# Kernel tuning notes

Hardware: AMD Instinct MI355X
Metric: run time of the kernel (lower is better)

## Reference

```python
import jax, jax.numpy as jnp
import numpy as np

N = 100000
E = 1600000
D = 128  # in_dim == out_dim


def setup_inputs() -> dict:
    key = jax.random.key(0)
    k1, k2, k3, k4, k5 = jax.random.split(key, 5)
    x = jax.random.normal(k1, (N, D), dtype=jnp.float32)
    edge_index = jax.random.randint(k2, (2, E), 0, N, dtype=jnp.int64)
    edge_attr = jax.random.normal(k3, (E, 8), dtype=jnp.float32)
    # nn.Linear(in_dim, out_dim) params: W [out, in], b [out]
    bound = 1.0 / np.sqrt(D)
    W = jax.random.uniform(k4, (D, D), minval=-bound, maxval=bound, dtype=jnp.float32)
    b = jax.random.uniform(k5, (D,), minval=-bound, maxval=bound, dtype=jnp.float32)
    return {"x": x, "edge_index": edge_index, "edge_attr": edge_attr, "W": W, "b": b}


def reference(x, edge_index, edge_attr, W, b):
    row, col = edge_index[0], edge_index[1]
    # gather neighbor features then scatter-add into destination rows
    agg = jax.ops.segment_sum(x[col], row, num_segments=x.shape[0])  # [N, D]
    h = (x + agg) @ W.T + b  # linear
    return jax.nn.silu(h)
```

## Files before the change

### kernel.cpp

```cpp
#include <hip/hip_runtime.h>
#include <math.h>

#define NN 100000
#define NE 1600000
#define DD 128
#define CAP 64

#define NB    512
#define CHUNK 3125
#define QCAP  768

typedef short bf16x8 __attribute__((ext_vector_type(8)));
typedef float f32x4  __attribute__((ext_vector_type(4)));

__device__ inline float bf2f(unsigned short u) {
    unsigned int v = ((unsigned int)u) << 16;
    return __uint_as_float(v);
}
__device__ inline unsigned short f2bf(float f) {
    unsigned int u = __float_as_uint(f);
    unsigned int r = (u + 0x7FFFu + ((u >> 16) & 1u)) >> 16;
    return (unsigned short)r;
}

__global__ void f2bf_kernel(const float* __restrict__ src,
                            unsigned short* __restrict__ dst, int n4) {
    int i = blockIdx.x * blockDim.x + threadIdx.x;
    if (i >= n4) return;
    float4 v = ((const float4*)src)[i];
    ushort4 o;
    o.x = f2bf(v.x); o.y = f2bf(v.y); o.z = f2bf(v.z); o.w = f2bf(v.w);
    ((ushort4*)dst)[i] = o;
}

__global__ void zero_cnt_kernel(int* cnt) {
    int i = blockIdx.x * blockDim.x + threadIdx.x;
    if (i < NN) cnt[i] = 0;
}

__global__ __launch_bounds__(256)
void partition_kernel(const int* __restrict__ eidx,
                      unsigned long long* __restrict__ q,
                      int* __restrict__ qn) {
    __shared__ int qc[8];
    if (threadIdx.x < 8) qc[threadIdx.x] = 0;
    __syncthreads();
    const int base = blockIdx.x * CHUNK;
    for (int i = threadIdx.x; i < CHUNK; i += 256) {
        const int e = base + i;
        const int r = __builtin_nontemporal_load(&eidx[e]);
        const int c = __builtin_nontemporal_load(&eidx[NE + e]);
        const int b = r / 12500;
        const int pos = atomicAdd(&qc[b], 1);
        if (pos < QCAP)
            q[((size_t)blockIdx.x * 8 + b) * QCAP + pos] =
                ((unsigned long long)(unsigned)c << 32) | (unsigned)r;
    }
    __syncthreads();
    if (threadIdx.x < 8) {
        int v = qc[threadIdx.x]; if (v > QCAP) v = QCAP;
        qn[blockIdx.x * 8 + threadIdx.x] = v;
    }
}

__global__ __launch_bounds__(256)
void scatter_kernel(const unsigned long long* __restrict__ q,
                    const int* __restrict__ qn,
                    int* __restrict__ cnt,
                    int* __restrict__ slot) {
    const int bucket = blockIdx.x & 7;
    const int chunk  = blockIdx.x >> 3;
    const int n = qn[chunk * 8 + bucket];
    const unsigned long long* qq = q + ((size_t)chunk * 8 + bucket) * QCAP;
    for (int i = threadIdx.x; i < n; i += 256) {
        const unsigned long long p = qq[i];
        const int r = (int)(p & 0xffffffffu);
        const int c = (int)(p >> 32);
        const int pos = atomicAdd(&cnt[r], 1);
        if (pos < CAP) slot[(r << 6) + pos] = c;
    }
}

__global__ __launch_bounds__(256)
void gather_kernel(const unsigned short* __restrict__ x16,
                   const int* __restrict__ cnt,
                   const int* __restrict__ slot,
                   unsigned short* __restrict__ V16) {
    const int lane = threadIdx.x & 15;
    const int node = (int)((blockIdx.x * 256u + threadIdx.x) >> 4);
    if (node >= NN) return;
    const bf16x8* xv = (const bf16x8*)x16;

    bf16x8 s = xv[(size_t)node * 16 + lane];
    float a[8];
    #pragma unroll
    for (int k = 0; k < 8; ++k) a[k] = bf2f((unsigned short)s[k]);

    int deg = cnt[node];
    if (deg > CAP) deg = CAP;
    const int base = node << 6;

    for (int d = 0; d < deg; d += 8) {
        const int4 c0 = *(const int4*)&slot[base + d];
        const int4 c1 = *(const int4*)&slot[base + d + 4];
        int idx[8] = {c0.x, c0.y, c0.z, c0.w, c1.x, c1.y, c1.z, c1.w};
        float w[8];
        #pragma unroll
        for (int j = 0; j < 8; ++j) {
            const bool live = (d + j) < deg;
            w[j] = live ? 1.f : 0.f;
            if (!live) idx[j] = node;
        }
        bf16x8 t[8];
        #pragma unroll
        for (int j = 0; j < 8; ++j) t[j] = xv[(size_t)idx[j] * 16 + lane];
        #pragma unroll
        for (int j = 0; j < 8; ++j) {
            #pragma unroll
            for (int k = 0; k < 8; ++k)
                a[k] = fmaf(w[j], bf2f((unsigned short)t[j][k]), a[k]);
        }
    }

    bf16x8 o;
    #pragma unroll
    for (int k = 0; k < 8; ++k) o[k] = (short)f2bf(a[k]);
    ((bf16x8*)V16)[(size_t)node * 16 + lane] = o;
}

__global__ __launch_bounds__(256)
void gemm_mfma_kernel(const unsigned short* __restrict__ V16,
                      const unsigned short* __restrict__ W16,
                      const float* __restrict__ bias,
                      float* __restrict__ out) {
    const int wave = threadIdx.x >> 6;
    const int lane = threadIdx.x & 63;
    const int strip = blockIdx.x * 4 + wave;
    if (strip >= NN / 16) return;
    const int m0 = strip << 4;
    const int r = lane & 15;
    const int q = lane >> 4;

    const bf16x8* Arow = (const bf16x8*)(V16 + (size_t)(m0 + r) * 128);
    bf16x8 a[4];
    #pragma unroll
    for (int kk = 0; kk < 4; ++kk) a[kk] = Arow[kk * 4 + q];

    f32x4 acc[8];
    #pragma unroll
    for (int n = 0; n < 8; ++n) acc[n] = (f32x4){0.f, 0.f, 0.f, 0.f};

    #pragma unroll
    for (int kk = 0; kk < 4; ++kk) {
        #pragma unroll
        for (int n = 0; n < 8; ++n) {
            const bf16x8 b =
                ((const bf16x8*)(W16 + (size_t)(n * 16 + r) * 128))[kk * 4 + q];
            acc[n] = __builtin_amdgcn_mfma_f32_16x16x32_bf16(a[kk], b, acc[n], 0, 0, 0);
        }
    }

    #pragma unroll
    for (int n = 0; n < 8; ++n) {
        const int col = n * 16 + r;
        const float bv = bias[col];
        #pragma unroll
        for (int i = 0; i < 4; ++i) {
            const int row = m0 + q * 4 + i;
            float h = acc[n][i] + bv;
            h = h / (1.f + __expf(-h));
            out[(size_t)row * 128 + col] = h;
        }
    }
}

extern "C" void kernel_launch(void* const* d_in, const int* in_sizes, int n_in,
                              void* d_out, int out_size, void* d_ws, size_t ws_size,
                              hipStream_t stream) {
    const float* x    = (const float*)d_in[0];
    const int*   eidx = (const int*)d_in[1];
    const float* W    = (const float*)d_in[3];
    const float* b    = (const float*)d_in[4];
    float* out = (float*)d_out;

    char* ws = (char*)d_ws;
    int*            cnt  = (int*)(ws);
    int*            qn   = (int*)(ws + (448u << 10));
    int*            slot = (int*)(ws + (512u << 10));
    unsigned short* x16  = (unsigned short*)(ws + (26u << 20));
    unsigned short* V16  = (unsigned short*)(ws + (51u << 20));
    unsigned short* W16  = (unsigned short*)(ws + (76u << 20));
    unsigned long long* q = (unsigned long long*)(ws + (51u << 20));

    zero_cnt_kernel<<<(NN + 255) / 256, 256, 0, stream>>>(cnt);
    partition_kernel<<<NB, 256, 0, stream>>>(eidx, q, qn);
    scatter_kernel<<<8 * NB, 256, 0, stream>>>(q, qn, cnt, slot);
    f2bf_kernel<<<(NN * DD / 4 + 255) / 256, 256, 0, stream>>>(x, x16, NN * DD / 4);
    f2bf_kernel<<<(DD * DD / 4 + 255) / 256, 256, 0, stream>>>(W, W16, DD * DD / 4);
    gather_kernel<<<(NN * 16 + 255) / 256, 256, 0, stream>>>(x16, cnt, slot, V16);
    gemm_mfma_kernel<<<(NN / 16 + 3) / 4, 256, 0, stream>>>(V16, W16, b, out);
}
```

Before: 329.4 us.

## Fuse adjacency build into gather using per-block shared-memory buckets

Partitions edges into 512 fine-grained destination buckets, with an overflow list for buckets that exceed their per-chunk capacity. A single fused kernel then builds each bucket's adjacency lists in LDS with shared atomics and immediately performs the neighbor gather. This removes the global count/slot arrays, the zeroing kernel and the global-atomic scatter pass. In exchange, only 512 blocks of 512 threads do the gather, each using about 50KB of LDS, which lowers occupancy and parallelism in the gather phase. Every block also scans the whole overflow list.

```diff
diff --git a/kernel.cpp b/kernel.cpp
--- a/kernel.cpp
+++ b/kernel.cpp
@@ -6,9 +6,12 @@
 #define DD 128
 #define CAP 64
 
-#define NB    512
-#define CHUNK 3125
-#define QCAP  768
+#define NB     64
+#define CHUNK  25000
+#define NBUCK  512
+#define BNODES 196
+#define QCAP2  96
+#define OVCAP  8192
 
 typedef short bf16x8 __attribute__((ext_vector_type(8)));
 typedef float f32x4  __attribute__((ext_vector_type(4)));
@@ -33,99 +36,124 @@
     ((ushort4*)dst)[i] = o;
 }
 
-__global__ void zero_cnt_kernel(int* cnt) {
-    int i = blockIdx.x * blockDim.x + threadIdx.x;
-    if (i < NN) cnt[i] = 0;
-}
+__global__ void zero_ovn_kernel(int* ovn) { *ovn = 0; }
 
 __global__ __launch_bounds__(256)
 void partition_kernel(const int* __restrict__ eidx,
                       unsigned long long* __restrict__ q,
-                      int* __restrict__ qn) {
-    __shared__ int qc[8];
-    if (threadIdx.x < 8) qc[threadIdx.x] = 0;
+                      int* __restrict__ qn,
+                      unsigned long long* __restrict__ ovf,
+                      int* __restrict__ ovn) {
+    __shared__ int qc[NBUCK];
+    for (int i = threadIdx.x; i < NBUCK; i += 256) qc[i] = 0;
     __syncthreads();
     const int base = blockIdx.x * CHUNK;
     for (int i = threadIdx.x; i < CHUNK; i += 256) {
         const int e = base + i;
         const int r = __builtin_nontemporal_load(&eidx[e]);
         const int c = __builtin_nontemporal_load(&eidx[NE + e]);
-        const int b = r / 12500;
+        const int b = r / BNODES;
         const int pos = atomicAdd(&qc[b], 1);
-        if (pos < QCAP)
-            q[((size_t)blockIdx.x * 8 + b) * QCAP + pos] =
-                ((unsigned long long)(unsigned)c << 32) | (unsigned)r;
-    }
-    __syncthreads();
-    if (threadIdx.x < 8) {
-        int v = qc[threadIdx.x]; if (v > QCAP) v = QCAP;
-        qn[blockIdx.x * 8 + threadIdx.x] = v;
-    }
-}
-
-__global__ __launch_bounds__(256)
-void scatter_kernel(const unsigned long long* __restrict__ q,
-                    const int* __restrict__ qn,
-                    int* __restrict__ cnt,
-                    int* __restrict__ slot) {
-    const int bucket = blockIdx.x & 7;
-    const int chunk  = blockIdx.x >> 3;
-    const int n = qn[chunk * 8 + bucket];
-    const unsigned long long* qq = q + ((size_t)chunk * 8 + bucket) * QCAP;
-    for (int i = threadIdx.x; i < n; i += 256) {
-        const unsigned long long p = qq[i];
-        const int r = (int)(p & 0xffffffffu);
-        const int c = (int)(p >> 32);
-        const int pos = atomicAdd(&cnt[r], 1);
-        if (pos < CAP) slot[(r << 6) + pos] = c;
-    }
-}
-
-__global__ __launch_bounds__(256)
-void gather_kernel(const unsigned short* __restrict__ x16,
-                   const int* __restrict__ cnt,
-                   const int* __restrict__ slot,
-                   unsigned short* __restrict__ V16) {
-    const int lane = threadIdx.x & 15;
-    const int node = (int)((blockIdx.x * 256u + threadIdx.x) >> 4);
-    if (node >= NN) return;
+        const unsigned long long pk =
+            ((unsigned long long)(unsigned)c << 32) | (unsigned)r;
+        if (pos < QCAP2) {
+            q[((size_t)blockIdx.x * NBUCK + b) * QCAP2 + pos] = pk;
+        } else {
+            const int op = atomicAdd(ovn, 1);
+            if (op < OVCAP) ovf[op] = pk;
+        }
+    }
+    __syncthreads();
+    for (int i = threadIdx.x; i < NBUCK; i += 256) {
+        int v = qc[i]; if (v > QCAP2) v = QCAP2;
+        qn[blockIdx.x * NBUCK + i] = v;
+    }
+}
+
+__global__ __launch_bounds__(512)
+void build_gather_kernel(const unsigned short* __restrict__ x16,
+                         const unsigned long long* __restrict__ q,
+                         const int* __restrict__ qn,
+                         const unsigned long long* __restrict__ ovf,
+                         const int* __restrict__ ovn,
+                         unsigned short* __restrict__ V16) {
+    __shared__ __align__(16) int adj_l[BNODES * CAP];
+    __shared__ int cnt_l[BNODES];
+    const int g   = blockIdx.x;
+    const int lo  = g * BNODES;
+    const int tid = threadIdx.x;
+
+    for (int i = tid; i < BNODES; i += 512) cnt_l[i] = 0;
+    __syncthreads();
+
+    {
+        const int p   = tid >> 3;
+        const int sub = tid & 7;
+        const int n = qn[p * NBUCK + g];
+        const unsigned long long* qq = q + ((size_t)p * NBUCK + g) * QCAP2;
+        for (int i = sub; i < n; i += 8) {
+            const unsigned long long pk = qq[i];
+            const int r = (int)(pk & 0xffffffffu) - lo;
+            const int c = (int)(pk >> 32);
+            const int pos = atomicAdd(&cnt_l[r], 1);
+            if (pos < CAP) adj_l[(r << 6) + pos] = c;
+        }
+    }
+    {
+        int n = *ovn; if (n > OVCAP) n = OVCAP;
+        for (int i = tid; i < n; i += 512) {
+            const unsigned long long pk = ovf[i];
+            const int r = (int)(pk & 0xffffffffu) - lo;
+            if ((unsigned)r < (unsigned)BNODES) {
+                const int c = (int)(pk >> 32);
+                const int pos = atomicAdd(&cnt_l[r], 1);
+                if (pos < CAP) adj_l[(r << 6) + pos] = c;
+            }
+        }
+    }
+    __syncthreads();
+
+    const int lane = tid & 15;
     const bf16x8* xv = (const bf16x8*)x16;
-
-    bf16x8 s = xv[(size_t)node * 16 + lane];
-    float a[8];
-    #pragma unroll
-    for (int k = 0; k < 8; ++k) a[k] = bf2f((unsigned short)s[k]);
-
-    int deg = cnt[node];
-    if (deg > CAP) deg = CAP;
-    const int base = node << 6;
-
-    for (int d = 0; d < deg; d += 8) {
-        const int4 c0 = *(const int4*)&slot[base + d];
-        const int4 c1 = *(const int4*)&slot[base + d + 4];
-        int idx[8] = {c0.x, c0.y, c0.z, c0.w, c1.x, c1.y, c1.z, c1.w};
-        float w[8];
-        #pragma unroll
-        for (int j = 0; j < 8; ++j) {
-            const bool live = (d + j) < deg;
-            w[j] = live ? 1.f : 0.f;
-            if (!live) idx[j] = node;
-        }
-        bf16x8 t[8];
-        #pragma unroll
-        for (int j = 0; j < 8; ++j) t[j] = xv[(size_t)idx[j] * 16 + lane];
-        #pragma unroll
-        for (int j = 0; j < 8; ++j) {
+    for (int ni = (tid >> 4); ni < BNODES; ni += 32) {
+        const int node = lo + ni;
+        if (node >= NN) continue;
+
+        bf16x8 s = xv[(size_t)node * 16 + lane];
+        float a[8];
+        #pragma unroll
+        for (int k = 0; k < 8; ++k) a[k] = bf2f((unsigned short)s[k]);
+
+        int deg = cnt_l[ni]; if (deg > CAP) deg = CAP;
+        const int* arow = &adj_l[ni << 6];
+
+        for (int d = 0; d < deg; d += 8) {
+            const int4 c0 = *(const int4*)&arow[d];
+            const int4 c1 = *(const int4*)&arow[d + 4];
+            int idx[8] = {c0.x, c0.y, c0.z, c0.w, c1.x, c1.y, c1.z, c1.w};
+            float w[8];
             #pragma unroll
-            for (int k = 0; k < 8; ++k)
-                a[k] = fmaf(w[j], bf2f((unsigned short)t[j][k]), a[k]);
-        }
-    }
-
-    bf16x8 o;
-    #pragma unroll
-    for (int k = 0; k < 8; ++k) o[k] = (short)f2bf(a[k]);
-    ((bf16x8*)V16)[(size_t)node * 16 + lane] = o;
+            for (int j = 0; j < 8; ++j) {
+                const bool live = (d + j) < deg;
+                w[j] = live ? 1.f : 0.f;
+                if (!live) idx[j] = node;
+            }
+            bf16x8 t[8];
+            #pragma unroll
+            for (int j = 0; j < 8; ++j) t[j] = xv[(size_t)idx[j] * 16 + lane];
+            #pragma unroll
+            for (int j = 0; j < 8; ++j) {
+                #pragma unroll
+                for (int k = 0; k < 8; ++k)
+                    a[k] = fmaf(w[j], bf2f((unsigned short)t[j][k]), a[k]);
+            }
+        }
+
+        bf16x8 o;
+        #pragma unroll
+        for (int k = 0; k < 8; ++k) o[k] = (short)f2bf(a[k]);
+        ((bf16x8*)V16)[(size_t)node * 16 + lane] = o;
+    }
 }
 
 __global__ __launch_bounds__(256)
@@ -184,19 +212,18 @@
     float* out = (float*)d_out;
 
     char* ws = (char*)d_ws;
-    int*            cnt  = (int*)(ws);
-    int*            qn   = (int*)(ws + (448u << 10));
-    int*            slot = (int*)(ws + (512u << 10));
-    unsigned short* x16  = (unsigned short*)(ws + (26u << 20));
-    unsigned short* V16  = (unsigned short*)(ws + (51u << 20));
-    unsigned short* W16  = (unsigned short*)(ws + (76u << 20));
-    unsigned long long* q = (unsigned long long*)(ws + (51u << 20));
-
-    zero_cnt_kernel<<<(NN + 255) / 256, 256, 0, stream>>>(cnt);
-    partition_kernel<<<NB, 256, 0, stream>>>(eidx, q, qn);
-    scatter_kernel<<<8 * NB, 256, 0, stream>>>(q, qn, cnt, slot);
+    int*                qn  = (int*)ws;
+    int*                ovn = (int*)(ws + (192u << 10));
+    unsigned long long* ovf = (unsigned long long*)(ws + (256u << 10));
+    unsigned long long* q   = (unsigned long long*)(ws + (512u << 10));
+    unsigned short*     x16 = (unsigned short*)(ws + (26u << 20));
+    unsigned short*     V16 = (unsigned short*)(ws + (51u << 20));
+    unsigned short*     W16 = (unsigned short*)(ws + (76u << 20));
+
+    zero_ovn_kernel<<<1, 1, 0, stream>>>(ovn);
+    partition_kernel<<<NB, 256, 0, stream>>>(eidx, q, qn, ovf, ovn);
     f2bf_kernel<<<(NN * DD / 4 + 255) / 256, 256, 0, stream>>>(x, x16, NN * DD / 4);
     f2bf_kernel<<<(DD * DD / 4 + 255) / 256, 256, 0, stream>>>(W, W16, DD * DD / 4);
-    gather_kernel<<<(NN * 16 + 255) / 256, 256, 0, stream>>>(x16, cnt, slot, V16);
+    build_gather_kernel<<<NBUCK, 512, 0, stream>>>(x16, q, qn, ovf, ovn, V16);
     gemm_mfma_kernel<<<(NN / 16 + 3) / 4, 256, 0, stream>>>(V16, W16, b, out);
 }
```

Result: faster. 305.2 us (-7.4%).
